# Optimization experiments

Hardware: AMD Instinct MI355X
Metric: run time of the kernel (lower is better)

The kernel has to match this reference:

```python
import jax, jax.numpy as jnp
import numpy as np


def setup_inputs() -> dict:
    key = jax.random.key(0)
    ks = jax.random.split(key, 32)
    def rn(i, shape, s=0.02):
        return jax.random.normal(ks[i], shape, dtype=jnp.float32) * s
    z = lambda n: jnp.zeros((n,), dtype=jnp.float32)
    return {
        'c2': rn(0, (8, 256, 112, 112), 1.0),
        'c3': rn(1, (8, 512, 56, 56), 1.0),
        'c4': rn(2, (8, 1024, 28, 28), 1.0),
        'c5': rn(3, (8, 2048, 14, 14), 1.0),
        'lat_w0': rn(4, (256, 256)),  'lat_b0': z(256),
        'lat_w1': rn(5, (512, 256)),  'lat_b1': z(256),
        'lat_w2': rn(6, (1024, 256)), 'lat_b2': z(256),
        'lat_w3': rn(7, (2048, 256)), 'lat_b3': z(256),
        'sp_w1': rn(8, (2048, 512)), 'sp_b1': z(512),
        'sp_w2': rn(9, (512, 4)),    'sp_b2': z(4),
        'qkv_w': rn(10, (256, 768)), 'qkv_b': z(768),
        'proj_w': rn(11, (256, 256)), 'proj_b': z(256),
        'gat_W': rn(12, (4, 256, 256)),
        'gat_a': rn(13, (4, 512)),
        'out_w': rn(14, (1024, 256)), 'out_b': z(256),
        'label_emb': rn(15, (80, 256), 1.0),
        'spec_w1': rn(16, (256, 128)), 'spec_b1': z(128),
        'spec_w2': rn(17, (128, 80)),  'spec_b2': z(80),
        'spat_w1': rn(18, (256, 128)), 'spat_b1': z(128),
        'spat_w2': rn(19, (128, 80)),  'spat_b2': z(80),
        'gate_w': rn(20, (256, 80)), 'gate_b': z(80),
        'unc_w': rn(21, (256, 80)),  'unc_b': z(80),
    }


def _forward(c2, c3, c4, c5,
             lat_w0, lat_b0, lat_w1, lat_b1, lat_w2, lat_b2, lat_w3, lat_b3,
             sp_w1, sp_b1, sp_w2, sp_b2,
             qkv_w, qkv_b, proj_w, proj_b,
             gat_W, gat_a, out_w, out_b, label_emb,
             spec_w1, spec_b1, spec_w2, spec_b2,
             spat_w1, spat_b1, spat_w2, spat_b2,
             gate_w, gate_b, unc_w, unc_b):
    B = c2.shape[0]
    L = label_emb.shape[0]
    C = 256
    # --- DynamicScaleAwareFPN ---
    pooled = c5.mean(axis=(2, 3))                                   # [B,2048]
    sw = jax.nn.softmax(jax.nn.relu(pooled @ sp_w1 + sp_b1) @ sp_w2 + sp_b2, axis=1)  # [B,4]
    H, W = c2.shape[2], c2.shape[3]
    feats = (c2, c3, c4, c5)
    lws = (lat_w0, lat_w1, lat_w2, lat_w3)
    lbs = (lat_b0, lat_b1, lat_b2, lat_b3)
    fused = jnp.zeros((B, C, H, W), dtype=c2.dtype)
    for i in range(4):  # fixed 4 scales
        l = jnp.einsum('bchw,cd->bdhw', feats[i], lws[i]) + lbs[i][None, :, None, None]
        if l.shape[2] != H or l.shape[3] != W:
            l = jax.image.resize(l, (B, C, H, W), method='bilinear')  # align_corners=False
        fused = fused + l * sw[:, i, None, None, None]
    # --- DeformableAttention (N=H*W > max_tokens=196 -> adaptive pool to 14x14) ---
    th = 14
    x = fused.reshape(B, C, th, H // th, th, W // th).mean(axis=(3, 5))  # exact adaptive avg pool
    x = x.reshape(B, C, th * th).transpose(0, 2, 1)                      # [B,196,C]
    N, nh, hd = th * th, 8, C // 8
    qkv = (x @ qkv_w + qkv_b).reshape(B, N, 3, nh, hd).transpose(2, 0, 3, 1, 4)
    q, k, v = qkv[0], qkv[1], qkv[2]                                     # [B,nh,N,hd]
    attn = jax.nn.softmax(jnp.einsum('bhnd,bhmd->bhnm', q, k) * (hd ** -0.5), axis=-1)
    xo = jnp.einsum('bhnm,bhmd->bhnd', attn, v).transpose(0, 2, 1, 3).reshape(B, N, C)
    xo = xo @ proj_w + proj_b
    gctx = xo.mean(axis=1)                                               # [B,C]
    # --- CrossLabelSemanticGraph (4 GAT heads) ---
    lf = label_emb[None] + gctx[:, None, :]                              # [B,L,C]
    def gat(Wm, avec):
        Wx = lf @ Wm                                                     # [B,L,C]
        # a([Wx_i ; Wx_j]) = Wx_i @ a1 + Wx_j @ a2  (avoids O(L^2*2C) tensor)
        s1 = Wx @ avec[:C]                                               # [B,L]
        s2 = Wx @ avec[C:]                                               # [B,L]
        e = jax.nn.leaky_relu(s1[:, :, None] + s2[:, None, :], 0.2)      # [B,L,L]
        att = jax.nn.softmax(e, axis=2)
        return att @ Wx, att
    heads, atts = jax.vmap(gat)(gat_W, gat_a)                            # [4,B,L,C],[4,B,L,L]
    concat = jnp.moveaxis(heads, 0, 2).reshape(B, L, 4 * C)              # head-order concat
    graph = concat @ out_w + out_b                                       # [B,L,C]
    agg = graph.mean(axis=1)                                             # [B,C]
    # --- SpectralSpatialFusion (dropout inactive at eval) ---
    spec = jax.nn.relu(agg @ spec_w1 + spec_b1) @ spec_w2 + spec_b2
    spat = jax.nn.relu(agg @ spat_w1 + spat_b1) @ spat_w2 + spat_b2
    gate = jax.nn.sigmoid(agg @ gate_w + gate_b)
    logits = gate * spec + (1.0 - gate) * spat
    # --- UncertaintyHead ---
    alpha = jax.nn.softplus(agg @ unc_w + unc_b) + 1.0
    unc = L / jnp.sum(alpha, axis=1, keepdims=True)
    return (logits, spec, spat, gate, unc, sw, atts)


def reference(c2, c3, c4, c5,
              lat_w0, lat_b0, lat_w1, lat_b1, lat_w2, lat_b2, lat_w3, lat_b3,
              sp_w1, sp_b1, sp_w2, sp_b2,
              qkv_w, qkv_b, proj_w, proj_b,
              gat_W, gat_a, out_w, out_b, label_emb,
              spec_w1, spec_b1, spec_w2, spec_b2,
              spat_w1, spat_b1, spat_w2, spat_b2,
              gate_w, gate_b, unc_w, unc_b):
    return _forward(c2, c3, c4, c5,
                    lat_w0, lat_b0, lat_w1, lat_b1, lat_w2, lat_b2, lat_w3, lat_b3,
                    sp_w1, sp_b1, sp_w2, sp_b2,
                    qkv_w, qkv_b, proj_w, proj_b,
                    gat_W, gat_a, out_w, out_b, label_emb,
                    spec_w1, spec_b1, spec_w2, spec_b2,
                    spat_w1, spat_b1, spat_w2, spat_b2,
                    gate_w, gate_b, unc_w, unc_b)
```

## Files before the change

kernel.cpp:

```cpp
#include <hip/hip_runtime.h>
#include <math.h>

typedef __attribute__((ext_vector_type(8))) short bshort8;
typedef __attribute__((ext_vector_type(4))) float f32x4;

#define DI __device__ __forceinline__

DI unsigned short f2bf(float x) {
    unsigned int u = __builtin_bit_cast(unsigned int, x);
    u += 0x7fffu + ((u >> 16) & 1u);
    return (unsigned short)(u >> 16);
}

DI bshort8 pack8(const float* v) {
    bshort8 r;
    #pragma unroll
    for (int j = 0; j < 8; j++) r[j] = (short)f2bf(v[j]);
    return r;
}

DI f32x4 mfma16(bshort8 a, bshort8 b, f32x4 c) {
    return __builtin_amdgcn_mfma_f32_16x16x32_bf16(a, b, c, 0, 0, 0);
}

__device__ const float W14[14][3] = {
    {0.875f, 0.125f, 0.f},
    {0.125f, 0.75f, 0.125f}, {0.125f, 0.75f, 0.125f}, {0.125f, 0.75f, 0.125f},
    {0.125f, 0.75f, 0.125f}, {0.125f, 0.75f, 0.125f}, {0.125f, 0.75f, 0.125f},
    {0.125f, 0.75f, 0.125f}, {0.125f, 0.75f, 0.125f}, {0.125f, 0.75f, 0.125f},
    {0.125f, 0.75f, 0.125f}, {0.125f, 0.75f, 0.125f}, {0.125f, 0.75f, 0.125f},
    {0.125f, 0.875f, 0.f}};
__device__ const float W28[14][4] = {
    {0.5f, 0.4375f, 0.0625f, 0.f},
    {0.0625f, 0.4375f, 0.4375f, 0.0625f}, {0.0625f, 0.4375f, 0.4375f, 0.0625f},
    {0.0625f, 0.4375f, 0.4375f, 0.0625f}, {0.0625f, 0.4375f, 0.4375f, 0.0625f},
    {0.0625f, 0.4375f, 0.4375f, 0.0625f}, {0.0625f, 0.4375f, 0.4375f, 0.0625f},
    {0.0625f, 0.4375f, 0.4375f, 0.0625f}, {0.0625f, 0.4375f, 0.4375f, 0.0625f},
    {0.0625f, 0.4375f, 0.4375f, 0.0625f}, {0.0625f, 0.4375f, 0.4375f, 0.0625f},
    {0.0625f, 0.4375f, 0.4375f, 0.0625f}, {0.0625f, 0.4375f, 0.4375f, 0.0625f},
    {0.0625f, 0.4375f, 0.5f, 0.f}};
__device__ const float W56[14][6] = {
    {0.25f, 0.25f, 0.25f, 0.21875f, 0.03125f, 0.f},
    {0.03125f, 0.21875f, 0.25f, 0.25f, 0.21875f, 0.03125f},
    {0.03125f, 0.21875f, 0.25f, 0.25f, 0.21875f, 0.03125f},
    {0.03125f, 0.21875f, 0.25f, 0.25f, 0.21875f, 0.03125f},
    {0.03125f, 0.21875f, 0.25f, 0.25f, 0.21875f, 0.03125f},
    {0.03125f, 0.21875f, 0.25f, 0.25f, 0.21875f, 0.03125f},
    {0.03125f, 0.21875f, 0.25f, 0.25f, 0.21875f, 0.03125f},
    {0.03125f, 0.21875f, 0.25f, 0.25f, 0.21875f, 0.03125f},
    {0.03125f, 0.21875f, 0.25f, 0.25f, 0.21875f, 0.03125f},
    {0.03125f, 0.21875f, 0.25f, 0.25f, 0.21875f, 0.03125f},
    {0.03125f, 0.21875f, 0.25f, 0.25f, 0.21875f, 0.03125f},
    {0.03125f, 0.21875f, 0.25f, 0.25f, 0.21875f, 0.03125f},
    {0.03125f, 0.21875f, 0.25f, 0.25f, 0.21875f, 0.03125f},
    {0.03125f, 0.21875f, 0.25f, 0.25f, 0.25f, 0.f}};

template <int N, int C, int TAPS>
__global__ __launch_bounds__(256) void pool_elem(
    const float* __restrict__ src, float* __restrict__ dst)
{
    unsigned id = blockIdx.x * 256u + threadIdx.x;
    unsigned p = id / 196u;
    unsigned r = id - p * 196u;
    unsigned ti = r / 14u, tj = r - ti * 14u;
    unsigned b = p / C, cin = p - b * C;
    const float* plane = src + (size_t)p * (N * N);
    float acc = 0.f;
    if constexpr (N == 112) {
        const float4* p4 = (const float4*)(plane + (size_t)(ti * 8) * 112 + tj * 8);
        #pragma unroll
        for (int i = 0; i < 8; i++) {
            float4 u = p4[i * 28];
            float4 v = p4[i * 28 + 1];
            acc += (u.x + u.y) + (u.z + u.w) + (v.x + v.y) + (v.z + v.w);
        }
        acc *= (1.f / 64.f);
    } else {
        constexpr int STRIDE = N / 14;
        const float (*WT)[TAPS] = (N == 14) ? (const float (*)[TAPS])W14
                                : (N == 28) ? (const float (*)[TAPS])W28
                                            : (const float (*)[TAPS])W56;
        int hs = (int)(STRIDE * ti) - 1; if (hs < 0) hs = 0;
        int ws = (int)(STRIDE * tj) - 1; if (ws < 0) ws = 0;
        float wh[TAPS], ww[TAPS];
        #pragma unroll
        for (int i = 0; i < TAPS; i++) { wh[i] = WT[ti][i]; ww[i] = WT[tj][i]; }
        #pragma unroll
        for (int i = 0; i < TAPS; i++) {
            int hi = hs + i; if (hi > N - 1) hi = N - 1;
            const float* row = plane + (size_t)hi * N;
            float rs = 0.f;
            #pragma unroll
            for (int j = 0; j < TAPS; j++) {
                int wj = ws + j; if (wj > N - 1) wj = N - 1;
                rs += ww[j] * row[wj];
            }
            acc += wh[i] * rs;
        }
    }
    dst[(size_t)cin * 1568 + b * 196 + r] = acc;
}

__global__ __launch_bounds__(256) void c5_mean(
    const float* __restrict__ c5, float* __restrict__ pooled)
{
    int wid = threadIdx.x >> 6, lane = threadIdx.x & 63;
    int p = blockIdx.x * 4 + wid;
    const float* plane = c5 + (size_t)p * 196;
    float v = plane[lane] + plane[64 + lane] + plane[128 + lane];
    if (lane < 4) v += plane[192 + lane];
    #pragma unroll
    for (int off = 32; off > 0; off >>= 1) v += __shfl_xor(v, off, 64);
    if (lane == 0) pooled[p] = v * (1.f / 196.f);
}

__global__ __launch_bounds__(512) void sw_part(
    const float* __restrict__ pooled, const float* __restrict__ sp_w1,
    float* __restrict__ partial)
{
    int b = blockIdx.x, kc = blockIdx.y, t = threadIdx.x;
    __shared__ float ps[256];
    if (t < 256) ps[t] = pooled[b * 2048 + kc * 256 + t];
    __syncthreads();
    float acc = 0.f;
    const float* w = sp_w1 + (size_t)(kc * 256) * 512 + t;
    #pragma unroll 8
    for (int c = 0; c < 256; c++) acc += ps[c] * w[(size_t)c * 512];
    partial[((size_t)b * 8 + kc) * 512 + t] = acc;
}

__global__ __launch_bounds__(512) void sw_fin(
    const float* __restrict__ partial, const float* __restrict__ sp_b1,
    const float* __restrict__ sp_w2, const float* __restrict__ sp_b2,
    const float* __restrict__ lb0, const float* __restrict__ lb1,
    const float* __restrict__ lb2, const float* __restrict__ lb3,
    float* __restrict__ sw_out, float* __restrict__ beff)
{
    int b = blockIdx.x, t = threadIdx.x;
    __shared__ float h[512];
    __shared__ float s4s[4];
    __shared__ float swl[4];
    float a = sp_b1[t];
    #pragma unroll
    for (int kc = 0; kc < 8; kc++) a += partial[((size_t)b * 8 + kc) * 512 + t];
    h[t] = fmaxf(a, 0.f);
    __syncthreads();
    int wv = t >> 6, lane = t & 63;
    if (wv < 4) {
        float acc = 0.f;
        #pragma unroll
        for (int i = 0; i < 8; i++) {
            int idx = lane + 64 * i;
            acc += h[idx] * sp_w2[idx * 4 + wv];
        }
        #pragma unroll
        for (int off = 32; off > 0; off >>= 1) acc += __shfl_xor(acc, off, 64);
        if (lane == 0) s4s[wv] = acc + sp_b2[wv];
    }
    __syncthreads();
    if (t == 0) {
        float mx = fmaxf(fmaxf(s4s[0], s4s[1]), fmaxf(s4s[2], s4s[3]));
        float e0 = expf(s4s[0] - mx), e1 = expf(s4s[1] - mx);
        float e2 = expf(s4s[2] - mx), e3 = expf(s4s[3] - mx);
        float inv = 1.f / (e0 + e1 + e2 + e3);
        swl[0] = e0 * inv; swl[1] = e1 * inv; swl[2] = e2 * inv; swl[3] = e3 * inv;
        for (int o = 0; o < 4; o++) sw_out[b * 4 + o] = swl[o];
    }
    __syncthreads();
    if (t < 256)
        beff[b * 256 + t] = swl[0] * lb0[t] + swl[1] * lb1[t] + swl[2] * lb2[t] + swl[3] * lb3[t];
}

__global__ __launch_bounds__(256) void xtok_init(
    const float* __restrict__ beff, float* __restrict__ xtok)
{
    int m = blockIdx.x, c = threadIdx.x;
    xtok[(size_t)m * 256 + c] = beff[(m / 196) * 256 + c];
}

__global__ __launch_bounds__(256) void lateral_slice(
    const float* __restrict__ pf0, const float* __restrict__ pf1,
    const float* __restrict__ pf2, const float* __restrict__ pf3,
    const float* __restrict__ w0, const float* __restrict__ w1,
    const float* __restrict__ w2, const float* __restrict__ w3,
    const float* __restrict__ sw, float* __restrict__ xtok)
{
    const int sArr[8]    = {0, 1, 2, 2, 3, 3, 3, 3};
    const int koffArr[8] = {0, 0, 0, 512, 0, 512, 1024, 1536};
    const int klenArr[8] = {256, 512, 512, 512, 512, 512, 512, 512};
    int sl = blockIdx.y;
    int s = sArr[sl], koff = koffArr[sl], klen = klenArr[sl];
    const float* pf = (s == 0) ? pf0 : (s == 1) ? pf1 : (s == 2) ? pf2 : pf3;
    const float* W  = (s == 0) ? w0  : (s == 1) ? w1  : (s == 2) ? w2  : w3;

    int mt = blockIdx.x % 49, nt = blockIdx.x / 49;
    int m0 = mt * 32, n0 = nt * 64;
    __shared__ alignas(16) unsigned short As[1024];
    __shared__ alignas(16) unsigned short Bs[2048];
    int t = threadIdx.x, lane = t & 63, wid = t >> 6;
    int wm = wid >> 1, wn = wid & 1;
    f32x4 acc0 = {0, 0, 0, 0}, acc1 = {0, 0, 0, 0};

    int f = t & 63;
    int mA = m0 + ((t >> 6) & 1) * 16 + (f & 15);
    int kbA = (f >> 4) * 8;
    int nB = n0 + (t >> 6) * 16 + (f & 15);
    int kbB = (f >> 4) * 8;
    float swv = sw[(mA / 196) * 4 + s];

    float ar[8], br[8];
    auto loadA = [&](int k0) {
        if (t < 128) {
            const float* base = pf + (size_t)(koff + k0 + kbA) * 1568 + mA;
            #pragma unroll
            for (int j = 0; j < 8; j++) ar[j] = base[(size_t)j * 1568] * swv;
        }
    };
    auto loadB = [&](int k0) {
        const float* base = W + (size_t)(koff + k0 + kbB) * 256 + nB;
        #pragma unroll
        for (int j = 0; j < 8; j++) br[j] = base[(size_t)j * 256];
    };

    loadA(0); loadB(0);
    for (int k0 = 0; k0 < klen; k0 += 32) {
        if (t < 128) *(bshort8*)&As[(((t >> 6) & 1) * 512 + f * 8)] = pack8(ar);
        *(bshort8*)&Bs[((t >> 6) * 512 + f * 8)] = pack8(br);
        __syncthreads();
        if (k0 + 32 < klen) { loadA(k0 + 32); loadB(k0 + 32); }
        bshort8 av = *(const bshort8*)&As[wm * 512 + lane * 8];
        bshort8 bv0 = *(const bshort8*)&Bs[(wn * 2 + 0) * 512 + lane * 8];
        bshort8 bv1 = *(const bshort8*)&Bs[(wn * 2 + 1) * 512 + lane * 8];
        acc0 = mfma16(av, bv0, acc0);
        acc1 = mfma16(av, bv1, acc1);
        __syncthreads();
    }
    int col0 = n0 + wn * 32 + (lane & 15);
    int rbase = m0 + wm * 16 + ((lane >> 4) << 2);
    #pragma unroll
    for (int r = 0; r < 4; r++) {
        int m = rbase + r;
        atomicAdd(&xtok[(size_t)m * 256 + col0], acc0[r]);
        atomicAdd(&xtok[(size_t)m * 256 + col0 + 16], acc1[r]);
    }
}

template <bool B_IS_KXN>
__global__ __launch_bounds__(256) void gemm_kernel(
    const float* __restrict__ Ab, int lda, long long sAy, long long sAz,
    const float* __restrict__ Bb, int ldb, long long sBy, long long sBz,
    float* __restrict__ Cb, int ldc, long long sCy, long long sCz,
    const float* __restrict__ bias, int M, int N, int K,
    float alpha, int mtiles)
{
    const float* A = Ab + blockIdx.y * sAy + blockIdx.z * sAz;
    const float* B = Bb + blockIdx.y * sBy + blockIdx.z * sBz;
    float* C = Cb + blockIdx.y * sCy + blockIdx.z * sCz;
    int mt = blockIdx.x % mtiles, nt = blockIdx.x / mtiles;
    int m0 = mt * 32, n0 = nt * 64;
    __shared__ alignas(16) unsigned short As[1024];
    __shared__ alignas(16) unsigned short Bs[2048];
    int t = threadIdx.x, lane = t & 63, wid = t >> 6;
    int wm = wid >> 1, wn = wid & 1;
    f32x4 acc0 = {0, 0, 0, 0}, acc1 = {0, 0, 0, 0};

    int f = t & 63;
    int mA = m0 + ((t >> 6) & 1) * 16 + (f & 15);
    int kbA = (f >> 4) * 8;
    int nB = n0 + (t >> 6) * 16 + (f & 15);
    int kbB = (f >> 4) * 8;

    float ar[8], br[8];
    auto loadA = [&](int k0) {
        if (t < 128) {
            int kb = k0 + kbA;
            if (mA < M && kb + 8 <= K) {
                const float4* p = (const float4*)(A + (size_t)mA * lda + kb);
                float4 u = p[0], v = p[1];
                ar[0] = u.x; ar[1] = u.y; ar[2] = u.z; ar[3] = u.w;
                ar[4] = v.x; ar[5] = v.y; ar[6] = v.z; ar[7] = v.w;
            } else {
                #pragma unroll
                for (int j = 0; j < 8; j++) {
                    int k = kb + j;
                    ar[j] = (mA < M && k < K) ? A[(size_t)mA * lda + k] : 0.f;
                }
            }
        }
    };
    auto loadB = [&](int k0) {
        int kb = k0 + kbB;
        if constexpr (B_IS_KXN) {
            #pragma unroll
            for (int j = 0; j < 8; j++) {
                int k = kb + j;
                br[j] = (k < K && nB < N) ? B[(size_t)k * ldb + nB] : 0.f;
            }
        } else {
            if (nB < N && kb + 8 <= K) {
                const float4* p = (const float4*)(B + (size_t)nB * ldb + kb);
                float4 u = p[0], v = p[1];
                br[0] = u.x; br[1] = u.y; br[2] = u.z; br[3] = u.w;
                br[4] = v.x; br[5] = v.y; br[6] = v.z; br[7] = v.w;
            } else {
                #pragma unroll
                for (int j = 0; j < 8; j++) {
                    int k = kb + j;
                    br[j] = (nB < N && k < K) ? B[(size_t)nB * ldb + k] : 0.f;
                }
            }
        }
    };

    loadA(0); loadB(0);
    for (int k0 = 0; k0 < K; k0 += 32) {
        if (t < 128) *(bshort8*)&As[(((t >> 6) & 1) * 512 + f * 8)] = pack8(ar);
        *(bshort8*)&Bs[((t >> 6) * 512 + f * 8)] = pack8(br);
        __syncthreads();
        if (k0 + 32 < K) { loadA(k0 + 32); loadB(k0 + 32); }
        bshort8 av = *(const bshort8*)&As[wm * 512 + lane * 8];
        bshort8 bv0 = *(const bshort8*)&Bs[(wn * 2 + 0) * 512 + lane * 8];
        bshort8 bv1 = *(const bshort8*)&Bs[(wn * 2 + 1) * 512 + lane * 8];
        acc0 = mfma16(av, bv0, acc0);
        acc1 = mfma16(av, bv1, acc1);
        __syncthreads();
    }
    int col0 = n0 + wn * 32 + (lane & 15);
    int rbase = m0 + wm * 16 + ((lane >> 4) << 2);
    #pragma unroll
    for (int r = 0; r < 4; r++) {
        int m = rbase + r;
        if (m < M) {
            if (col0 < N) {
                float v = acc0[r] * alpha;
                if (bias) v += bias[col0];
                C[(size_t)m * ldc + col0] = v;
            }
            int c1 = col0 + 16;
            if (c1 < N) {
                float v = acc1[r] * alpha;
                if (bias) v += bias[c1];
                C[(size_t)m * ldc + c1] = v;
            }
        }
    }
}

__global__ __launch_bounds__(256) void attn_softmax(float* __restrict__ S)
{
    int wid = threadIdx.x >> 6, lane = threadIdx.x & 63;
    size_t row = (size_t)blockIdx.x * 4 + wid;
    float* p = S + row * 196;
    float v0 = p[lane];
    float v1 = p[64 + lane];
    float v2 = p[128 + lane];
    float v3 = (lane < 4) ? p[192 + lane] : -1e30f;
    float mx = fmaxf(fmaxf(v0, v1), fmaxf(v2, v3));
    #pragma unroll
    for (int off = 32; off > 0; off >>= 1) mx = fmaxf(mx, __shfl_xor(mx, off, 64));
    float e0 = expf(v0 - mx), e1 = expf(v1 - mx), e2 = expf(v2 - mx);
    float e3 = (lane < 4) ? expf(v3 - mx) : 0.f;
    float sum = e0 + e1 + e2 + e3;
    #pragma unroll
    for (int off = 32; off > 0; off >>= 1) sum += __shfl_xor(sum, off, 64);
    float inv = 1.f / sum;
    p[lane] = e0 * inv;
    p[64 + lane] = e1 * inv;
    p[128 + lane] = e2 * inv;
    if (lane < 4) p[192 + lane] = e3 * inv;
}

__global__ __launch_bounds__(256) void xo_part(
    const float* __restrict__ xo, float* __restrict__ xopart)
{
    int b = blockIdx.x, g = blockIdx.y, t = threadIdx.x;
    const float* base = xo + ((size_t)b * 196 + g * 28) * 256 + t;
    float s = 0.f;
    #pragma unroll
    for (int n = 0; n < 28; n++) s += base[(size_t)n * 256];
    xopart[(b * 7 + g) * 256 + t] = s;
}

__global__ __launch_bounds__(256) void gctx_part(
    const float* __restrict__ xopart, const float* __restrict__ proj_w,
    float* __restrict__ gpart)
{
    int b = blockIdx.x, kc = blockIdx.y, t = threadIdx.x;
    __shared__ float xm[64];
    if (t < 64) {
        float s = 0.f;
        #pragma unroll
        for (int g = 0; g < 7; g++) s += xopart[(b * 7 + g) * 256 + kc * 64 + t];
        xm[t] = s * (1.f / 196.f);
    }
    __syncthreads();
    float acc = 0.f;
    const float* w = proj_w + (size_t)(kc * 64) * 256 + t;
    #pragma unroll 8
    for (int j = 0; j < 64; j++) acc += xm[j] * w[(size_t)j * 256];
    gpart[(b * 4 + kc) * 256 + t] = acc;
}

__global__ __launch_bounds__(256) void wa2(
    const float* __restrict__ gat_W, const float* __restrict__ gat_a,
    float* __restrict__ Wa)
{
    int h = blockIdx.x, q = blockIdx.y;
    int t = threadIdx.x, w = t >> 6, lane = t & 63;
    __shared__ float a1[256], a2[256];
    a1[t] = gat_a[h * 512 + t];
    a2[t] = gat_a[h * 512 + 256 + t];
    __syncthreads();
    for (int ci = 0; ci < 16; ci++) {
        int c = q * 64 + w * 16 + ci;
        const float* row = gat_W + (size_t)h * 65536 + (size_t)c * 256;
        float p1 = 0.f, p2 = 0.f;
        #pragma unroll
        for (int jj = 0; jj < 4; jj++) {
            float v = row[lane + 64 * jj];
            p1 += v * a1[lane + 64 * jj];
            p2 += v * a2[lane + 64 * jj];
        }
        #pragma unroll
        for (int off = 32; off > 0; off >>= 1) {
            p1 += __shfl_xor(p1, off, 64);
            p2 += __shfl_xor(p2, off, 64);
        }
        if (lane == 0) { Wa[h * 512 + c] = p1; Wa[h * 512 + 256 + c] = p2; }
    }
}

__global__ __launch_bounds__(256) void lf_s12(
    const float* __restrict__ gpart, const float* __restrict__ proj_b,
    const float* __restrict__ lemb, const float* __restrict__ Wa,
    float* __restrict__ lf, float* __restrict__ s12)
{
    int l = blockIdx.x, b = blockIdx.y, t = threadIdx.x;
    int w = t >> 6, lane = t & 63;
    __shared__ float row[256];
    float g = proj_b[t] + gpart[(b * 4 + 0) * 256 + t] + gpart[(b * 4 + 1) * 256 + t]
            + gpart[(b * 4 + 2) * 256 + t] + gpart[(b * 4 + 3) * 256 + t];
    float v = lemb[l * 256 + t] + g;
    lf[((size_t)b * 80 + l) * 256 + t] = v;
    row[t] = v;
    __syncthreads();
    #pragma unroll
    for (int pp = 0; pp < 2; pp++) {
        int pair = w * 2 + pp;
        float p = 0.f;
        #pragma unroll
        for (int jj = 0; jj < 4; jj++) {
            int c = lane + 64 * jj;
            p += row[c] * Wa[pair * 256 + c];
        }
        #pragma unroll
        for (int off = 32; off > 0; off >>= 1) p += __shfl_xor(p, off, 64);
        if (lane == 0) s12[(b * 8 + pair) * 80 + l] = p;
    }
}

__global__ __launch_bounds__(256) void gat_rows(
    const float* __restrict__ s12, float* __restrict__ atts)
{
    int b = blockIdx.x, h = blockIdx.y, z = blockIdx.z;
    int t = threadIdx.x, w = t >> 6, lane = t & 63;
    int i = z * 4 + w;
    float s1i = s12[(b * 8 + h * 2) * 80 + i];
    const float* s2 = s12 + (b * 8 + h * 2 + 1) * 80;
    float v0 = s1i + s2[lane]; v0 = v0 > 0.f ? v0 : 0.2f * v0;
    float v1 = -1e30f;
    if (lane < 16) { v1 = s1i + s2[64 + lane]; v1 = v1 > 0.f ? v1 : 0.2f * v1; }
    float mx = fmaxf(v0, v1);
    #pragma unroll
    for (int off = 32; off > 0; off >>= 1) mx = fmaxf(mx, __shfl_xor(mx, off, 64));
    float e0 = expf(v0 - mx), e1 = (lane < 16) ? expf(v1 - mx) : 0.f;
    float sum = e0 + e1;
    #pragma unroll
    for (int off = 32; off > 0; off >>= 1) sum += __shfl_xor(sum, off, 64);
    float inv = 1.f / sum;
    float* orow = atts + (size_t)h * 51200 + b * 6400 + i * 80;
    orow[lane] = e0 * inv;
    if (lane < 16) orow[64 + lane] = e1 * inv;
}

__global__ __launch_bounds__(256) void amlf_kernel(
    const float* __restrict__ atts, const float* __restrict__ lf,
    float* __restrict__ amlf)
{
    int b = blockIdx.x, h = blockIdx.y, t = threadIdx.x;
    __shared__ float am[80];
    if (t < 80) {
        const float* base = atts + (size_t)h * 51200 + b * 6400 + t;
        float acc = 0.f;
        #pragma unroll 8
        for (int l = 0; l < 80; l++) acc += base[l * 80];
        am[t] = acc * (1.f / 80.f);
    }
    __syncthreads();
    float acc = 0.f;
    const float* lfb = lf + (size_t)b * 80 * 256 + t;
    #pragma unroll 8
    for (int l = 0; l < 80; l++) acc += am[l] * lfb[(size_t)l * 256];
    amlf[(b * 4 + h) * 256 + t] = acc;
}

__global__ __launch_bounds__(256) void hm_part(
    const float* __restrict__ amlf, const float* __restrict__ gat_W,
    float* __restrict__ hmpart)
{
    int b = blockIdx.x, h = blockIdx.y, kc = blockIdx.z, t = threadIdx.x;
    __shared__ float av[64];
    if (t < 64) av[t] = amlf[(b * 4 + h) * 256 + kc * 64 + t];
    __syncthreads();
    float acc = 0.f;
    const float* w = gat_W + (size_t)h * 65536 + (size_t)(kc * 64) * 256 + t;
    #pragma unroll 8
    for (int j = 0; j < 64; j++) acc += av[j] * w[(size_t)j * 256];
    hmpart[((b * 4 + h) * 4 + kc) * 256 + t] = acc;
}

__global__ __launch_bounds__(256) void as_part(
    const float* __restrict__ hmpart, const float* __restrict__ out_w,
    float* __restrict__ aspart)
{
    int b = blockIdx.x, kc = blockIdx.y, t = threadIdx.x;
    __shared__ float hv[64];
    if (t < 64) {
        int hk = kc * 64 + t;
        int h = hk >> 8, c = hk & 255;
        const float* p = hmpart + ((size_t)(b * 4 + h) * 4) * 256 + c;
        hv[t] = p[0] + p[256] + p[512] + p[768];
    }
    __syncthreads();
    float acc = 0.f;
    const float* w = out_w + (size_t)(kc * 64) * 256 + t;
    #pragma unroll 8
    for (int j = 0; j < 64; j++) acc += hv[j] * w[(size_t)j * 256];
    aspart[(b * 16 + kc) * 256 + t] = acc;
}

__global__ __launch_bounds__(256) void as_fin(
    const float* __restrict__ aspart, const float* __restrict__ out_b,
    float* __restrict__ a_s)
{
    int b = blockIdx.x, t = threadIdx.x;
    float acc = out_b[t];
    #pragma unroll
    for (int kc = 0; kc < 16; kc++) acc += aspart[(b * 16 + kc) * 256 + t];
    a_s[b * 256 + t] = acc;
}

__global__ __launch_bounds__(256) void mlp1(
    const float* __restrict__ a_s,
    const float* __restrict__ spec_w1, const float* __restrict__ spec_b1,
    const float* __restrict__ spat_w1, const float* __restrict__ spat_b1,
    float* __restrict__ hbuf)
{
    int b = blockIdx.x, which = blockIdx.y, t = threadIdx.x;
    const float* w1 = which ? spat_w1 : spec_w1;
    const float* b1 = which ? spat_b1 : spec_b1;
    __shared__ float as_s[256];
    __shared__ float red[256];
    as_s[t] = a_s[b * 256 + t];
    __syncthreads();
    int o = t & 63, ks = t >> 6;
    #pragma unroll
    for (int p = 0; p < 2; p++) {
        int oo = p * 64 + o;
        float acc = 0.f;
        const float* w = w1 + (size_t)(ks * 64) * 128 + oo;
        #pragma unroll 8
        for (int j = 0; j < 64; j++) acc += as_s[ks * 64 + j] * w[(size_t)j * 128];
        red[t] = acc;
        __syncthreads();
        if (ks == 0) {
            float v = red[o] + red[64 + o] + red[128 + o] + red[192 + o] + b1[oo];
            hbuf[(b * 2 + which) * 128 + oo] = fmaxf(v, 0.f);
        }
        __syncthreads();
    }
}

__global__ __launch_bounds__(256) void mlp2(
    const float* __restrict__ a_s, const float* __restrict__ hbuf,
    const float* __restrict__ spec_w2, const float* __restrict__ spec_b2,
    const float* __restrict__ spat_w2, const float* __restrict__ spat_b2,
    const float* __restrict__ gate_w, const float* __restrict__ gate_b,
    const float* __restrict__ unc_w, const float* __restrict__ unc_b,
    float* __restrict__ fv)
{
    int b = blockIdx.x, head = blockIdx.y, t = threadIdx.x;
    __shared__ float src[256];
    __shared__ float red[240];
    const float* w; const float* bias; int K;
    if (head == 0)      { w = spec_w2; bias = spec_b2; K = 128; }
    else if (head == 1) { w = spat_w2; bias = spat_b2; K = 128; }
    else if (head == 2) { w = gate_w; bias = gate_b; K = 256; }
    else                { w = unc_w;  bias = unc_b;  K = 256; }
    if (head < 2) { if (t < 128) src[t] = hbuf[(b * 2 + head) * 128 + t]; }
    else src[t] = a_s[b * 256 + t];
    __syncthreads();
    if (t < 240) {
        int o = t % 80, s = t / 80;
        int k0 = (K * s) / 3, k1 = (K * (s + 1)) / 3;
        float acc = 0.f;
        #pragma unroll 8
        for (int k = k0; k < k1; k++) acc += src[k] * w[(size_t)k * 80 + o];
        red[t] = acc;
    }
    __syncthreads();
    if (t < 80) fv[(b * 4 + head) * 80 + t] = red[t] + red[80 + t] + red[160 + t] + bias[t];
}

__global__ __launch_bounds__(128) void final_comb(
    const float* __restrict__ fv, float* __restrict__ out)
{
    int b = blockIdx.x, t = threadIdx.x;
    __shared__ float alph[80];
    if (t < 80) {
        float sp = fv[(b * 4 + 0) * 80 + t], st = fv[(b * 4 + 1) * 80 + t];
        float gz = fv[(b * 4 + 2) * 80 + t], uz = fv[(b * 4 + 3) * 80 + t];
        float g = 1.f / (1.f + expf(-gz));
        out[b * 80 + t] = g * sp + (1.f - g) * st;
        out[640 + b * 80 + t] = sp;
        out[1280 + b * 80 + t] = st;
        out[1920 + b * 80 + t] = g;
        alph[t] = log1pf(expf(uz)) + 1.f;
    }
    __syncthreads();
    if (t == 0) {
        float s = 0.f;
        for (int l = 0; l < 80; l++) s += alph[l];
        out[2560 + b] = 80.f / s;
    }
}

extern "C" void kernel_launch(void* const* d_in, const int* in_sizes, int n_in,
                              void* d_out, int out_size, void* d_ws, size_t ws_size,
                              hipStream_t stream)
{
    (void)in_sizes; (void)n_in; (void)out_size; (void)ws_size;
    const float* c2 = (const float*)d_in[0];
    const float* c3 = (const float*)d_in[1];
    const float* c4 = (const float*)d_in[2];
    const float* c5 = (const float*)d_in[3];
    const float* lat_w0 = (const float*)d_in[4];
    const float* lat_b0 = (const float*)d_in[5];
    const float* lat_w1 = (const float*)d_in[6];
    const float* lat_b1 = (const float*)d_in[7];
    const float* lat_w2 = (const float*)d_in[8];
    const float* lat_b2 = (const float*)d_in[9];
    const float* lat_w3 = (const float*)d_in[10];
    const float* lat_b3 = (const float*)d_in[11];
    const float* sp_w1 = (const float*)d_in[12];
    const float* sp_b1 = (const float*)d_in[13];
    const float* sp_w2 = (const float*)d_in[14];
    const float* sp_b2 = (const float*)d_in[15];
    const float* qkv_w = (const float*)d_in[16];
    const float* qkv_b = (const float*)d_in[17];
    const float* proj_w = (const float*)d_in[18];
    const float* proj_b = (const float*)d_in[19];
    const float* gat_W = (const float*)d_in[20];
    const float* gat_a = (const float*)d_in[21];
    const float* out_w = (const float*)d_in[22];
    const float* out_b = (const float*)d_in[23];
    const float* label_emb = (const float*)d_in[24];
    const float* spec_w1 = (const float*)d_in[25];
    const float* spec_b1 = (const float*)d_in[26];
    const float* spec_w2 = (const float*)d_in[27];
    const float* spec_b2 = (const float*)d_in[28];
    const float* spat_w1 = (const float*)d_in[29];
    const float* spat_b1 = (const float*)d_in[30];
    const float* spat_w2 = (const float*)d_in[31];
    const float* spat_b2 = (const float*)d_in[32];
    const float* gate_w = (const float*)d_in[33];
    const float* gate_b = (const float*)d_in[34];
    const float* unc_w = (const float*)d_in[35];
    const float* unc_b = (const float*)d_in[36];

    float* out = (float*)d_out;
    float* ws = (float*)d_ws;

    float* pf0    = ws + 0;
    float* pf1    = ws + 401408;
    float* pf2    = ws + 1204224;
    float* pf3    = ws + 2809856;
    float* pooled = ws + 6021120;
    float* beff   = ws + 6037504;
    float* swpart = ws + 6039552;
    float* qkv    = ws + 0;
    float* S      = ws + 1204224;
    float* xo     = ws + 3662848;
    float* lf     = ws + 4064256;
    float* Wa     = ws + 4228096;
    float* xopart = ws + 4230144;
    float* gpart  = ws + 4244480;
    float* s12    = ws + 4252672;
    float* amlf   = ws + 4257792;
    float* hmpart = ws + 4265984;
    float* aspart = ws + 4298752;
    float* a_sb   = ws + 4331520;
    float* hbuf   = ws + 4333568;
    float* fv     = ws + 4335616;
    float* xtok   = ws + 6106112;

    float* swp  = out + 2568;
    float* atts = out + 2600;

    pool_elem<112, 256, 8><<<1568, 256, 0, stream>>>(c2, pf0);
    pool_elem<56, 512, 6><<<3136, 256, 0, stream>>>(c3, pf1);
    pool_elem<28, 1024, 4><<<6272, 256, 0, stream>>>(c4, pf2);
    pool_elem<14, 2048, 3><<<12544, 256, 0, stream>>>(c5, pf3);
    c5_mean<<<4096, 256, 0, stream>>>(c5, pooled);
    sw_part<<<dim3(8, 8), 512, 0, stream>>>(pooled, sp_w1, swpart);
    sw_fin<<<8, 512, 0, stream>>>(swpart, sp_b1, sp_w2, sp_b2,
                                  lat_b0, lat_b1, lat_b2, lat_b3, swp, beff);
    xtok_init<<<1568, 256, 0, stream>>>(beff, xtok);
    lateral_slice<<<dim3(196, 8), 256, 0, stream>>>(pf0, pf1, pf2, pf3,
                                                    lat_w0, lat_w1, lat_w2, lat_w3,
                                                    swp, xtok);
    gemm_kernel<true><<<dim3(49 * 12, 1, 1), 256, 0, stream>>>(
        xtok, 256, 0, 0, qkv_w, 768, 0, 0, qkv, 768, 0, 0,
        qkv_b, 1568, 768, 256, 1.f, 49);
    gemm_kernel<false><<<dim3(7 * 4, 8, 8), 256, 0, stream>>>(
        qkv, 768, 150528, 32, qkv + 256, 768, 150528, 32,
        S, 196, 307328, 38416, nullptr, 196, 196, 32, 0.17677669529663687f, 7);
    attn_softmax<<<3136, 256, 0, stream>>>(S);
    gemm_kernel<true><<<dim3(7, 8, 8), 256, 0, stream>>>(
        S, 196, 307328, 38416, qkv + 512, 768, 150528, 32,
        xo, 256, 50176, 32, nullptr, 196, 32, 196, 1.f, 7);
    xo_part<<<dim3(8, 7), 256, 0, stream>>>(xo, xopart);
    gctx_part<<<dim3(8, 4), 256, 0, stream>>>(xopart, proj_w, gpart);
    wa2<<<dim3(4, 4), 256, 0, stream>>>(gat_W, gat_a, Wa);
    lf_s12<<<dim3(80, 8), 256, 0, stream>>>(gpart, proj_b, label_emb, Wa, lf, s12);
    gat_rows<<<dim3(8, 4, 20), 256, 0, stream>>>(s12, atts);
    amlf_kernel<<<dim3(8, 4), 256, 0, stream>>>(atts, lf, amlf);
    hm_part<<<dim3(8, 4, 4), 256, 0, stream>>>(amlf, gat_W, hmpart);
    as_part<<<dim3(8, 16), 256, 0, stream>>>(hmpart, out_w, aspart);
    as_fin<<<8, 256, 0, stream>>>(aspart, out_b, a_sb);
    mlp1<<<dim3(8, 2), 256, 0, stream>>>(a_sb, spec_w1, spec_b1, spat_w1, spat_b1, hbuf);
    mlp2<<<dim3(8, 4), 256, 0, stream>>>(a_sb, hbuf,
        spec_w2, spec_b2, spat_w2, spat_b2,
        gate_w, gate_b, unc_w, unc_b, fv);
    final_comb<<<8, 128, 0, stream>>>(fv, out);
}
```

Baseline: 487.2 us.

## Merge pooling launches and fuse tail kernels into one grid-synced persistent kernel

Combines the four pooling kernels and the c5 mean into one launch, folds the xtok bias broadcast into sw_fin, and replaces about twelve small tail kernels with a single 640-block kernel that uses atomic-counter grid barriers between stages. amlf and hm_part are also merged, and as_fin, mlp1, mlp2 and final_comb become one per-batch body. The aim is to remove launch overhead and idle gaps between many tiny dependent kernels. In exchange it relies on all 640 blocks being resident at once, since otherwise the spin barrier can deadlock, and some stages now run with fewer blocks.

```diff
diff --git a/kernel.cpp b/kernel.cpp
--- a/kernel.cpp
+++ b/kernel.cpp
@@ -56,10 +56,10 @@
     {0.03125f, 0.21875f, 0.25f, 0.25f, 0.25f, 0.f}};
 
 template <int N, int C, int TAPS>
-__global__ __launch_bounds__(256) void pool_elem(
-    const float* __restrict__ src, float* __restrict__ dst)
-{
-    unsigned id = blockIdx.x * 256u + threadIdx.x;
+DI void pool_body(const float* __restrict__ src, float* __restrict__ dst,
+                  unsigned blk, unsigned t)
+{
+    unsigned id = blk * 256u + t;
     unsigned p = id / 196u;
     unsigned r = id - p * 196u;
     unsigned ti = r / 14u, tj = r - ti * 14u;
@@ -101,17 +101,33 @@
     dst[(size_t)cin * 1568 + b * 196 + r] = acc;
 }
 
-__global__ __launch_bounds__(256) void c5_mean(
-    const float* __restrict__ c5, float* __restrict__ pooled)
-{
-    int wid = threadIdx.x >> 6, lane = threadIdx.x & 63;
-    int p = blockIdx.x * 4 + wid;
+DI void c5_mean_body(const float* __restrict__ c5, float* __restrict__ pooled,
+                     unsigned blk, unsigned t)
+{
+    int wid = t >> 6, lane = t & 63;
+    int p = blk * 4 + wid;
     const float* plane = c5 + (size_t)p * 196;
     float v = plane[lane] + plane[64 + lane] + plane[128 + lane];
     if (lane < 4) v += plane[192 + lane];
     #pragma unroll
     for (int off = 32; off > 0; off >>= 1) v += __shfl_xor(v, off, 64);
     if (lane == 0) pooled[p] = v * (1.f / 196.f);
+}
+
+__global__ __launch_bounds__(256) void pool_all(
+    const float* __restrict__ c2, const float* __restrict__ c3,
+    const float* __restrict__ c4, const float* __restrict__ c5,
+    float* __restrict__ pf0, float* __restrict__ pf1,
+    float* __restrict__ pf2, float* __restrict__ pf3,
+    float* __restrict__ pooled, unsigned* __restrict__ bar)
+{
+    unsigned bx = blockIdx.x, t = threadIdx.x;
+    if (bx == 27615u && t < 8u) bar[t] = 0u;
+    if (bx < 1568u)       pool_body<112, 256, 8>(c2, pf0, bx, t);
+    else if (bx < 4704u)  pool_body<56, 512, 6>(c3, pf1, bx - 1568u, t);
+    else if (bx < 10976u) pool_body<28, 1024, 4>(c4, pf2, bx - 4704u, t);
+    else if (bx < 23520u) pool_body<14, 2048, 3>(c5, pf3, bx - 10976u, t);
+    else                  c5_mean_body(c5, pooled, bx - 23520u, t);
 }
 
 __global__ __launch_bounds__(512) void sw_part(
@@ -134,12 +150,13 @@
     const float* __restrict__ sp_w2, const float* __restrict__ sp_b2,
     const float* __restrict__ lb0, const float* __restrict__ lb1,
     const float* __restrict__ lb2, const float* __restrict__ lb3,
-    float* __restrict__ sw_out, float* __restrict__ beff)
+    float* __restrict__ sw_out, float* __restrict__ xtok)
 {
     int b = blockIdx.x, t = threadIdx.x;
     __shared__ float h[512];
     __shared__ float s4s[4];
     __shared__ float swl[4];
+    __shared__ float bf_s[256];
     float a = sp_b1[t];
     #pragma unroll
     for (int kc = 0; kc < 8; kc++) a += partial[((size_t)b * 8 + kc) * 512 + t];
@@ -168,14 +185,12 @@
     }
     __syncthreads();
     if (t < 256)
-        beff[b * 256 + t] = swl[0] * lb0[t] + swl[1] * lb1[t] + swl[2] * lb2[t] + swl[3] * lb3[t];
-}
-
-__global__ __launch_bounds__(256) void xtok_init(
-    const float* __restrict__ beff, float* __restrict__ xtok)
-{
-    int m = blockIdx.x, c = threadIdx.x;
-    xtok[(size_t)m * 256 + c] = beff[(m / 196) * 256 + c];
+        bf_s[t] = swl[0] * lb0[t] + swl[1] * lb1[t] + swl[2] * lb2[t] + swl[3] * lb3[t];
+    __syncthreads();
+    int c = t & 255, half = t >> 8;
+    float bv = bf_s[c];
+    float* xb = xtok + (size_t)b * 196 * 256 + c;
+    for (int r = half; r < 196; r += 2) xb[(size_t)r * 256] = bv;
 }
 
 __global__ __launch_bounds__(256) void lateral_slice(
@@ -370,10 +385,21 @@
     if (lane < 4) p[192 + lane] = e3 * inv;
 }
 
-__global__ __launch_bounds__(256) void xo_part(
-    const float* __restrict__ xo, float* __restrict__ xopart)
-{
-    int b = blockIdx.x, g = blockIdx.y, t = threadIdx.x;
+
+DI void gsync(unsigned* c) {
+    __syncthreads();
+    if (threadIdx.x == 0) {
+        __threadfence();
+        atomicAdd(c, 1u);
+        while (atomicAdd(c, 0u) < 640u) __builtin_amdgcn_s_sleep(8);
+        __threadfence();
+    }
+    __syncthreads();
+}
+
+DI void xo_part_body(const float* __restrict__ xo, float* __restrict__ xopart,
+                     int b, int g, int t)
+{
     const float* base = xo + ((size_t)b * 196 + g * 28) * 256 + t;
     float s = 0.f;
     #pragma unroll
@@ -381,11 +407,36 @@
     xopart[(b * 7 + g) * 256 + t] = s;
 }
 
-__global__ __launch_bounds__(256) void gctx_part(
-    const float* __restrict__ xopart, const float* __restrict__ proj_w,
-    float* __restrict__ gpart)
-{
-    int b = blockIdx.x, kc = blockIdx.y, t = threadIdx.x;
+DI void wa2_body(const float* __restrict__ gat_W, const float* __restrict__ gat_a,
+                 float* __restrict__ Wa, int h, int q, int t)
+{
+    int w = t >> 6, lane = t & 63;
+    __shared__ float a1[256], a2[256];
+    a1[t] = gat_a[h * 512 + t];
+    a2[t] = gat_a[h * 512 + 256 + t];
+    __syncthreads();
+    for (int ci = 0; ci < 16; ci++) {
+        int c = q * 64 + w * 16 + ci;
+        const float* row = gat_W + (size_t)h * 65536 + (size_t)c * 256;
+        float p1 = 0.f, p2 = 0.f;
+        #pragma unroll
+        for (int jj = 0; jj < 4; jj++) {
+            float v = row[lane + 64 * jj];
+            p1 += v * a1[lane + 64 * jj];
+            p2 += v * a2[lane + 64 * jj];
+        }
+        #pragma unroll
+        for (int off = 32; off > 0; off >>= 1) {
+            p1 += __shfl_xor(p1, off, 64);
+            p2 += __shfl_xor(p2, off, 64);
+        }
+        if (lane == 0) { Wa[h * 512 + c] = p1; Wa[h * 512 + 256 + c] = p2; }
+    }
+}
+
+DI void gctx_part_body(const float* __restrict__ xopart, const float* __restrict__ proj_w,
+                       float* __restrict__ gpart, int b, int kc, int t)
+{
     __shared__ float xm[64];
     if (t < 64) {
         float s = 0.f;
@@ -401,41 +452,11 @@
     gpart[(b * 4 + kc) * 256 + t] = acc;
 }
 
-__global__ __launch_bounds__(256) void wa2(
-    const float* __restrict__ gat_W, const float* __restrict__ gat_a,
-    float* __restrict__ Wa)
-{
-    int h = blockIdx.x, q = blockIdx.y;
-    int t = threadIdx.x, w = t >> 6, lane = t & 63;
-    __shared__ float a1[256], a2[256];
-    a1[t] = gat_a[h * 512 + t];
-    a2[t] = gat_a[h * 512 + 256 + t];
-    __syncthreads();
-    for (int ci = 0; ci < 16; ci++) {
-        int c = q * 64 + w * 16 + ci;
-        const float* row = gat_W + (size_t)h * 65536 + (size_t)c * 256;
-        float p1 = 0.f, p2 = 0.f;
-        #pragma unroll
-        for (int jj = 0; jj < 4; jj++) {
-            float v = row[lane + 64 * jj];
-            p1 += v * a1[lane + 64 * jj];
-            p2 += v * a2[lane + 64 * jj];
-        }
-        #pragma unroll
-        for (int off = 32; off > 0; off >>= 1) {
-            p1 += __shfl_xor(p1, off, 64);
-            p2 += __shfl_xor(p2, off, 64);
-        }
-        if (lane == 0) { Wa[h * 512 + c] = p1; Wa[h * 512 + 256 + c] = p2; }
-    }
-}
-
-__global__ __launch_bounds__(256) void lf_s12(
-    const float* __restrict__ gpart, const float* __restrict__ proj_b,
-    const float* __restrict__ lemb, const float* __restrict__ Wa,
-    float* __restrict__ lf, float* __restrict__ s12)
-{
-    int l = blockIdx.x, b = blockIdx.y, t = threadIdx.x;
+DI void lf_s12_body(const float* __restrict__ gpart, const float* __restrict__ proj_b,
+                    const float* __restrict__ lemb, const float* __restrict__ Wa,
+                    float* __restrict__ lf, float* __restrict__ s12,
+                    int l, int b, int t)
+{
     int w = t >> 6, lane = t & 63;
     __shared__ float row[256];
     float g = proj_b[t] + gpart[(b * 4 + 0) * 256 + t] + gpart[(b * 4 + 1) * 256 + t]
@@ -459,11 +480,10 @@
     }
 }
 
-__global__ __launch_bounds__(256) void gat_rows(
-    const float* __restrict__ s12, float* __restrict__ atts)
-{
-    int b = blockIdx.x, h = blockIdx.y, z = blockIdx.z;
-    int t = threadIdx.x, w = t >> 6, lane = t & 63;
+DI void gat_rows_body(const float* __restrict__ s12, float* __restrict__ atts,
+                      int b, int h, int z, int t)
+{
+    int w = t >> 6, lane = t & 63;
     int i = z * 4 + w;
     float s1i = s12[(b * 8 + h * 2) * 80 + i];
     const float* s2 = s12 + (b * 8 + h * 2 + 1) * 80;
@@ -483,12 +503,12 @@
     if (lane < 16) orow[64 + lane] = e1 * inv;
 }
 
-__global__ __launch_bounds__(256) void amlf_kernel(
-    const float* __restrict__ atts, const float* __restrict__ lf,
-    float* __restrict__ amlf)
-{
-    int b = blockIdx.x, h = blockIdx.y, t = threadIdx.x;
+DI void amlf_hm_body(const float* __restrict__ atts, const float* __restrict__ lf,
+                     const float* __restrict__ gat_W, float* __restrict__ hm,
+                     int b, int h, int t)
+{
     __shared__ float am[80];
+    __shared__ float av[256];
     if (t < 80) {
         const float* base = atts + (size_t)h * 51200 + b * 6400 + t;
         float acc = 0.f;
@@ -501,35 +521,23 @@
     const float* lfb = lf + (size_t)b * 80 * 256 + t;
     #pragma unroll 8
     for (int l = 0; l < 80; l++) acc += am[l] * lfb[(size_t)l * 256];
-    amlf[(b * 4 + h) * 256 + t] = acc;
-}
-
-__global__ __launch_bounds__(256) void hm_part(
-    const float* __restrict__ amlf, const float* __restrict__ gat_W,
-    float* __restrict__ hmpart)
-{
-    int b = blockIdx.x, h = blockIdx.y, kc = blockIdx.z, t = threadIdx.x;
-    __shared__ float av[64];
-    if (t < 64) av[t] = amlf[(b * 4 + h) * 256 + kc * 64 + t];
-    __syncthreads();
-    float acc = 0.f;
-    const float* w = gat_W + (size_t)h * 65536 + (size_t)(kc * 64) * 256 + t;
+    av[t] = acc;
+    __syncthreads();
+    float acc2 = 0.f;
+    const float* w = gat_W + (size_t)h * 65536 + t;
     #pragma unroll 8
-    for (int j = 0; j < 64; j++) acc += av[j] * w[(size_t)j * 256];
-    hmpart[((b * 4 + h) * 4 + kc) * 256 + t] = acc;
-}
-
-__global__ __launch_bounds__(256) void as_part(
-    const float* __restrict__ hmpart, const float* __restrict__ out_w,
-    float* __restrict__ aspart)
-{
-    int b = blockIdx.x, kc = blockIdx.y, t = threadIdx.x;
+    for (int k = 0; k < 256; k++) acc2 += av[k] * w[(size_t)k * 256];
+    hm[(b * 4 + h) * 256 + t] = acc2;
+}
+
+DI void as_part_body(const float* __restrict__ hm, const float* __restrict__ out_w,
+                     float* __restrict__ aspart, int b, int kc, int t)
+{
     __shared__ float hv[64];
     if (t < 64) {
         int hk = kc * 64 + t;
         int h = hk >> 8, c = hk & 255;
-        const float* p = hmpart + ((size_t)(b * 4 + h) * 4) * 256 + c;
-        hv[t] = p[0] + p[256] + p[512] + p[768];
+        hv[t] = hm[(b * 4 + h) * 256 + c];
     }
     __syncthreads();
     float acc = 0.f;
@@ -539,100 +547,107 @@
     aspart[(b * 16 + kc) * 256 + t] = acc;
 }
 
-__global__ __launch_bounds__(256) void as_fin(
-    const float* __restrict__ aspart, const float* __restrict__ out_b,
-    float* __restrict__ a_s)
-{
-    int b = blockIdx.x, t = threadIdx.x;
-    float acc = out_b[t];
-    #pragma unroll
-    for (int kc = 0; kc < 16; kc++) acc += aspart[(b * 16 + kc) * 256 + t];
-    a_s[b * 256 + t] = acc;
-}
-
-__global__ __launch_bounds__(256) void mlp1(
-    const float* __restrict__ a_s,
-    const float* __restrict__ spec_w1, const float* __restrict__ spec_b1,
-    const float* __restrict__ spat_w1, const float* __restrict__ spat_b1,
-    float* __restrict__ hbuf)
-{
-    int b = blockIdx.x, which = blockIdx.y, t = threadIdx.x;
-    const float* w1 = which ? spat_w1 : spec_w1;
-    const float* b1 = which ? spat_b1 : spec_b1;
+DI void fin_body(const float* __restrict__ aspart, const float* __restrict__ out_b,
+                 const float* __restrict__ spec_w1, const float* __restrict__ spec_b1,
+                 const float* __restrict__ spec_w2, const float* __restrict__ spec_b2,
+                 const float* __restrict__ spat_w1, const float* __restrict__ spat_b1,
+                 const float* __restrict__ spat_w2, const float* __restrict__ spat_b2,
+                 const float* __restrict__ gate_w, const float* __restrict__ gate_b,
+                 const float* __restrict__ unc_w, const float* __restrict__ unc_b,
+                 float* __restrict__ out, int b, int t)
+{
     __shared__ float as_s[256];
-    __shared__ float red[256];
-    as_s[t] = a_s[b * 256 + t];
-    __syncthreads();
-    int o = t & 63, ks = t >> 6;
-    #pragma unroll
-    for (int p = 0; p < 2; p++) {
-        int oo = p * 64 + o;
-        float acc = 0.f;
-        const float* w = w1 + (size_t)(ks * 64) * 128 + oo;
+    __shared__ float hb[256];
+    __shared__ float fvs[320];
+    float a = out_b[t];
+    #pragma unroll
+    for (int kc = 0; kc < 16; kc++) a += aspart[(b * 16 + kc) * 256 + t];
+    as_s[t] = a;
+    __syncthreads();
+    {
+        int which = t >> 7, oo = t & 127;
+        const float* w1 = which ? spat_w1 : spec_w1;
+        const float* b1 = which ? spat_b1 : spec_b1;
+        float acc = b1[oo];
         #pragma unroll 8
-        for (int j = 0; j < 64; j++) acc += as_s[ks * 64 + j] * w[(size_t)j * 128];
-        red[t] = acc;
-        __syncthreads();
-        if (ks == 0) {
-            float v = red[o] + red[64 + o] + red[128 + o] + red[192 + o] + b1[oo];
-            hbuf[(b * 2 + which) * 128 + oo] = fmaxf(v, 0.f);
-        }
-        __syncthreads();
-    }
-}
-
-__global__ __launch_bounds__(256) void mlp2(
-    const float* __restrict__ a_s, const float* __restrict__ hbuf,
-    const float* __restrict__ spec_w2, const float* __restrict__ spec_b2,
-    const float* __restrict__ spat_w2, const float* __restrict__ spat_b2,
-    const float* __restrict__ gate_w, const float* __restrict__ gate_b,
-    const float* __restrict__ unc_w, const float* __restrict__ unc_b,
-    float* __restrict__ fv)
-{
-    int b = blockIdx.x, head = blockIdx.y, t = threadIdx.x;
-    __shared__ float src[256];
-    __shared__ float red[240];
-    const float* w; const float* bias; int K;
-    if (head == 0)      { w = spec_w2; bias = spec_b2; K = 128; }
-    else if (head == 1) { w = spat_w2; bias = spat_b2; K = 128; }
-    else if (head == 2) { w = gate_w; bias = gate_b; K = 256; }
-    else                { w = unc_w;  bias = unc_b;  K = 256; }
-    if (head < 2) { if (t < 128) src[t] = hbuf[(b * 2 + head) * 128 + t]; }
-    else src[t] = a_s[b * 256 + t];
-    __syncthreads();
-    if (t < 240) {
-        int o = t % 80, s = t / 80;
-        int k0 = (K * s) / 3, k1 = (K * (s + 1)) / 3;
-        float acc = 0.f;
-        #pragma unroll 8
-        for (int k = k0; k < k1; k++) acc += src[k] * w[(size_t)k * 80 + o];
-        red[t] = acc;
-    }
-    __syncthreads();
-    if (t < 80) fv[(b * 4 + head) * 80 + t] = red[t] + red[80 + t] + red[160 + t] + bias[t];
-}
-
-__global__ __launch_bounds__(128) void final_comb(
-    const float* __restrict__ fv, float* __restrict__ out)
-{
-    int b = blockIdx.x, t = threadIdx.x;
-    __shared__ float alph[80];
+        for (int k = 0; k < 256; k++) acc += as_s[k] * w1[(size_t)k * 128 + oo];
+        hb[t] = fmaxf(acc, 0.f);
+    }
+    __syncthreads();
+    for (int oi = t; oi < 320; oi += 256) {
+        int head = oi / 80, o = oi - head * 80;
+        float acc;
+        if (head == 0) {
+            acc = spec_b2[o];
+            #pragma unroll 8
+            for (int k = 0; k < 128; k++) acc += hb[k] * spec_w2[(size_t)k * 80 + o];
+        } else if (head == 1) {
+            acc = spat_b2[o];
+            #pragma unroll 8
+            for (int k = 0; k < 128; k++) acc += hb[128 + k] * spat_w2[(size_t)k * 80 + o];
+        } else if (head == 2) {
+            acc = gate_b[o];
+            #pragma unroll 8
+            for (int k = 0; k < 256; k++) acc += as_s[k] * gate_w[(size_t)k * 80 + o];
+        } else {
+            acc = unc_b[o];
+            #pragma unroll 8
+            for (int k = 0; k < 256; k++) acc += as_s[k] * unc_w[(size_t)k * 80 + o];
+        }
+        fvs[oi] = acc;
+    }
+    __syncthreads();
     if (t < 80) {
-        float sp = fv[(b * 4 + 0) * 80 + t], st = fv[(b * 4 + 1) * 80 + t];
-        float gz = fv[(b * 4 + 2) * 80 + t], uz = fv[(b * 4 + 3) * 80 + t];
+        float sp = fvs[t], st = fvs[80 + t], gz = fvs[160 + t], uz = fvs[240 + t];
         float g = 1.f / (1.f + expf(-gz));
         out[b * 80 + t] = g * sp + (1.f - g) * st;
         out[640 + b * 80 + t] = sp;
         out[1280 + b * 80 + t] = st;
         out[1920 + b * 80 + t] = g;
-        alph[t] = log1pf(expf(uz)) + 1.f;
+        as_s[t] = log1pf(expf(uz)) + 1.f;
     }
     __syncthreads();
     if (t == 0) {
         float s = 0.f;
-        for (int l = 0; l < 80; l++) s += alph[l];
+        for (int l = 0; l < 80; l++) s += as_s[l];
         out[2560 + b] = 80.f / s;
     }
+}
+
+__global__ __launch_bounds__(256, 4) void tail_coop(
+    const float* __restrict__ xo, const float* __restrict__ proj_w,
+    const float* __restrict__ proj_b,
+    const float* __restrict__ gat_W, const float* __restrict__ gat_a,
+    const float* __restrict__ lemb,
+    const float* __restrict__ out_w, const float* __restrict__ out_b,
+    const float* __restrict__ spec_w1, const float* __restrict__ spec_b1,
+    const float* __restrict__ spec_w2, const float* __restrict__ spec_b2,
+    const float* __restrict__ spat_w1, const float* __restrict__ spat_b1,
+    const float* __restrict__ spat_w2, const float* __restrict__ spat_b2,
+    const float* __restrict__ gate_w, const float* __restrict__ gate_b,
+    const float* __restrict__ unc_w, const float* __restrict__ unc_b,
+    float* __restrict__ xopart, float* __restrict__ gpart, float* __restrict__ Wa,
+    float* __restrict__ lf, float* __restrict__ s12, float* __restrict__ atts,
+    float* __restrict__ hm, float* __restrict__ aspart, float* __restrict__ out,
+    unsigned* __restrict__ bar)
+{
+    int blk = blockIdx.x, t = threadIdx.x;
+    if (blk < 56) xo_part_body(xo, xopart, blk & 7, blk >> 3, t);
+    else if (blk < 72) wa2_body(gat_W, gat_a, Wa, (blk - 56) & 3, (blk - 56) >> 2, t);
+    gsync(bar + 0);
+    if (blk < 32) gctx_part_body(xopart, proj_w, gpart, blk & 7, blk >> 3, t);
+    gsync(bar + 1);
+    lf_s12_body(gpart, proj_b, lemb, Wa, lf, s12, blk % 80, blk / 80, t);
+    gsync(bar + 2);
+    gat_rows_body(s12, atts, blk & 7, (blk >> 3) & 3, blk >> 5, t);
+    gsync(bar + 3);
+    if (blk < 32) amlf_hm_body(atts, lf, gat_W, hm, blk & 7, blk >> 3, t);
+    gsync(bar + 4);
+    if (blk < 128) as_part_body(hm, out_w, aspart, blk & 7, blk >> 3, t);
+    gsync(bar + 5);
+    if (blk < 8) fin_body(aspart, out_b, spec_w1, spec_b1, spec_w2, spec_b2,
+                          spat_w1, spat_b1, spat_w2, spat_b2,
+                          gate_w, gate_b, unc_w, unc_b, out, blk, t);
 }
 
 extern "C" void kernel_launch(void* const* d_in, const int* in_sizes, int n_in,
@@ -686,7 +701,6 @@
     float* pf2    = ws + 1204224;
     float* pf3    = ws + 2809856;
     float* pooled = ws + 6021120;
-    float* beff   = ws + 6037504;
     float* swpart = ws + 6039552;
     float* qkv    = ws + 0;
     float* S      = ws + 1204224;
@@ -696,26 +710,18 @@
     float* xopart = ws + 4230144;
     float* gpart  = ws + 4244480;
     float* s12    = ws + 4252672;
-    float* amlf   = ws + 4257792;
-    float* hmpart = ws + 4265984;
+    float* hm     = ws + 4265984;
     float* aspart = ws + 4298752;
-    float* a_sb   = ws + 4331520;
-    float* hbuf   = ws + 4333568;
-    float* fv     = ws + 4335616;
     float* xtok   = ws + 6106112;
+    unsigned* bar = (unsigned*)(ws + 6507776);
 
     float* swp  = out + 2568;
     float* atts = out + 2600;
 
-    pool_elem<112, 256, 8><<<1568, 256, 0, stream>>>(c2, pf0);
-    pool_elem<56, 512, 6><<<3136, 256, 0, stream>>>(c3, pf1);
-    pool_elem<28, 1024, 4><<<6272, 256, 0, stream>>>(c4, pf2);
-    pool_elem<14, 2048, 3><<<12544, 256, 0, stream>>>(c5, pf3);
-    c5_mean<<<4096, 256, 0, stream>>>(c5, pooled);
+    pool_all<<<27616, 256, 0, stream>>>(c2, c3, c4, c5, pf0, pf1, pf2, pf3, pooled, bar);
     sw_part<<<dim3(8, 8), 512, 0, stream>>>(pooled, sp_w1, swpart);
     sw_fin<<<8, 512, 0, stream>>>(swpart, sp_b1, sp_w2, sp_b2,
-                                  lat_b0, lat_b1, lat_b2, lat_b3, swp, beff);
-    xtok_init<<<1568, 256, 0, stream>>>(beff, xtok);
+                                  lat_b0, lat_b1, lat_b2, lat_b3, swp, xtok);
     lateral_slice<<<dim3(196, 8), 256, 0, stream>>>(pf0, pf1, pf2, pf3,
                                                     lat_w0, lat_w1, lat_w2, lat_w3,
                                                     swp, xtok);
@@ -729,18 +735,10 @@
     gemm_kernel<true><<<dim3(7, 8, 8), 256, 0, stream>>>(
         S, 196, 307328, 38416, qkv + 512, 768, 150528, 32,
         xo, 256, 50176, 32, nullptr, 196, 32, 196, 1.f, 7);
-    xo_part<<<dim3(8, 7), 256, 0, stream>>>(xo, xopart);
-    gctx_part<<<dim3(8, 4), 256, 0, stream>>>(xopart, proj_w, gpart);
-    wa2<<<dim3(4, 4), 256, 0, stream>>>(gat_W, gat_a, Wa);
-    lf_s12<<<dim3(80, 8), 256, 0, stream>>>(gpart, proj_b, label_emb, Wa, lf, s12);
-    gat_rows<<<dim3(8, 4, 20), 256, 0, stream>>>(s12, atts);
-    amlf_kernel<<<dim3(8, 4), 256, 0, stream>>>(atts, lf, amlf);
-    hm_part<<<dim3(8, 4, 4), 256, 0, stream>>>(amlf, gat_W, hmpart);
-    as_part<<<dim3(8, 16), 256, 0, stream>>>(hmpart, out_w, aspart);
-    as_fin<<<8, 256, 0, stream>>>(aspart, out_b, a_sb);
-    mlp1<<<dim3(8, 2), 256, 0, stream>>>(a_sb, spec_w1, spec_b1, spat_w1, spat_b1, hbuf);
-    mlp2<<<dim3(8, 4), 256, 0, stream>>>(a_sb, hbuf,
-        spec_w2, spec_b2, spat_w2, spat_b2,
-        gate_w, gate_b, unc_w, unc_b, fv);
-    final_comb<<<8, 128, 0, stream>>>(fv, out);
-}
+    tail_coop<<<640, 256, 0, stream>>>(
+        xo, proj_w, proj_b, gat_W, gat_a, label_emb, out_w, out_b,
+        spec_w1, spec_b1, spec_w2, spec_b2,
+        spat_w1, spat_b1, spat_w2, spat_b2,
+        gate_w, gate_b, unc_w, unc_b,
+        xopart, gpart, Wa, lf, s12, atts, hm, aspart, out, bar);
+}
```

Result: slower. 778.9 us (+59.9%).
